# Kernel optimization log

Hardware: AMD Instinct MI355X
Metric: run time of the kernel (lower is better)

## Reference

```python
import jax, jax.numpy as jnp
import numpy as np

B = 524288      # batch
D = 16          # ds_dim
N = 32          # number of dynamical systems
H = 128         # gating hidden width


def setup_inputs() -> dict:
    key = jax.random.key(0)
    ks = jax.random.split(key, 8)
    x_cur = jax.random.normal(ks[0], (B, D), dtype=jnp.float32)
    W1 = jax.random.normal(ks[1], (H, D), dtype=jnp.float32) * 0.1
    b1 = jax.random.normal(ks[2], (H,), dtype=jnp.float32) * 0.1
    W2 = jax.random.normal(ks[3], (N, H), dtype=jnp.float32) * 0.1
    b2 = jax.random.normal(ks[4], (N,), dtype=jnp.float32) * 0.1
    # B matrices are PSD (geotorch.positive_semidefinite), C are skew-symmetric (geotorch.skew)
    Braw = jax.random.normal(ks[5], (N, D, D), dtype=jnp.float32) * 0.3
    B_mats = jnp.einsum('nij,nkj->nik', Braw, Braw)  # PSD: R R^T
    Craw = jax.random.normal(ks[6], (N, D, D), dtype=jnp.float32) * 0.3
    C_mats = 0.5 * (Craw - jnp.swapaxes(Craw, -1, -2))  # skew-symmetric
    x_target = jax.random.normal(ks[7], (1, D), dtype=jnp.float32)
    return {"x_cur": x_cur, "W1": W1, "b1": b1, "W2": W2, "b2": b2,
            "B_mats": B_mats, "C_mats": C_mats, "x_target": x_target}


def reference(x_cur, W1, b1, W2, b2, B_mats, C_mats, x_target):
    # gating weights: softmax(Linear -> ReLU -> Linear)
    h = jax.nn.relu(x_cur @ W1.T + b1)          # [B, H]
    w_all = jax.nn.softmax(h @ W2.T + b2, axis=1)  # [B, N]
    # per-system linear map A_i = B_i + C_i applied to (x* - x)
    A = B_mats + C_mats                          # [N, D, D]
    diff = x_target - x_cur                      # [B, D]
    # torch.mm(A, diff.T).T == diff @ A.T -> proj[b,n,k] = sum_d A[n,k,d] diff[b,d]
    proj = jnp.einsum('nkd,bd->bnk', A, diff)    # [B, N, D]
    out = jnp.einsum('bn,bnk->bk', w_all, proj)  # [B, D]
    return out
```

## Files before the change

kernel.cpp:

```cpp
#include <hip/hip_runtime.h>

#define BATCH 524288

typedef __bf16 bf16x8 __attribute__((ext_vector_type(8)));
typedef __bf16 bf16x2 __attribute__((ext_vector_type(2)));
typedef float f32x4 __attribute__((ext_vector_type(4)));
typedef float f32x8 __attribute__((ext_vector_type(8)));
typedef float f32x2 __attribute__((ext_vector_type(2)));

#define SW1 16384
#define SZC 20480
#define SW2 20512
#define SB2 28704
#define SXT 28832
#define SHC 28896
#define SMEM_BYTES (28896 + 4 * 2560)

__device__ __forceinline__ f32x8 load8(const float* __restrict__ p) {
    float4 a = *(const float4*)p;
    float4 b = *(const float4*)(p + 4);
    f32x8 v = {a.x, a.y, a.z, a.w, b.x, b.y, b.z, b.w};
    return v;
}

__device__ __forceinline__ int pack2bf(float a, float b) {
    f32x2 v = {a, b};
    bf16x2 p = __builtin_convertvector(v, bf16x2);
    return __builtin_bit_cast(int, p);
}

__global__ __launch_bounds__(256, 4) void andp_v10(
    const float* __restrict__ x_cur,
    const float* __restrict__ W1,
    const float* __restrict__ b1,
    const float* __restrict__ W2,
    const float* __restrict__ b2,
    const float* __restrict__ Bm,
    const float* __restrict__ Cm,
    const float* __restrict__ x_t,
    float* __restrict__ out)
{
    extern __shared__ char smem[];
    int* sA2i = (int*)smem;
    int* sW1i = (int*)(smem + SW1);
    int* sW2i = (int*)(smem + SW2);
    const int tid = threadIdx.x;

#pragma unroll
    for (int i = 0; i < 16; ++i) {
        int o2 = tid + i * 256;
        int o  = o2 * 2;
        int kk = o >> 9, qp = (o >> 7) & 3, k = (o >> 3) & 15, j = o & 7;
        int n = 2 * kk + (qp >> 1), d = (qp & 1) * 8 + j;
        int src = n * 256 + k * 16 + d;
        float2 bv = *(const float2*)(Bm + src);
        float2 cv = *(const float2*)(Cm + src);
        sA2i[o2] = pack2bf(bv.x + cv.x, bv.y + cv.y);
    }
#pragma unroll
    for (int i = 0; i < 4; ++i) {
        int o2 = tid + i * 256;
        int o  = o2 * 2;
        int t = o >> 8, qq = (o >> 7) & 1, cc = (o >> 3) & 15, j = o & 7;
        int src = (t * 16 + cc) * 16 + qq * 8 + j;
        float2 v = *(const float2*)(W1 + src);
        sW1i[o2] = pack2bf(v.x, v.y);
    }
    if (tid < 8) ((int*)(smem + SZC))[tid] = 0;
#pragma unroll
    for (int i = 0; i < 8; ++i) {
        int o2 = tid + i * 256;
        int chunk = o2 >> 8, rem = o2 & 255;
        int ln = rem >> 2, j2 = rem & 3;
        int qq = ln >> 4, cc = ln & 15;
        int t2 = chunk >> 2, s = chunk & 3;
        int src = (t2 * 16 + cc) * 128 + s * 32 + 4 * qq + j2;
        sW2i[o2] = pack2bf(W2[src], W2[src + 16]);
    }
    if (tid < 32) ((float*)(smem + SB2))[tid] = b2[tid];
    if (tid < 16) ((float*)(smem + SXT))[tid] = x_t[tid];

    const int wave = tid >> 6, lane = tid & 63;
    const int c = lane & 15, q = lane >> 4;
    const int qh = q >> 1;
    const int hh = (q & 1) * 8;
    const int c4 = c * 4;

    const char* sW1f = smem + SW1;
    const int w1base = (q < 2) ? ((q * 16 + c) * 16) : (SZC - SW1);
    const int w1step = (q < 2) ? 512 : 0;
    const char* sW2f = smem + SW2 + lane * 16;
    __bf16* hcw0 = (__bf16*)(smem + SHC + wave * 2560);
    __bf16* hcw1 = hcw0 + 640;
    const float* sB2f = (const float*)(smem + SB2);
    const float* sXTf = (const float*)(smem + SXT);

    float b1v[8];
#pragma unroll
    for (int t = 0; t < 8; ++t) b1v[t] = b1[t * 16 + c];

    __syncthreads();

    const int blk_row = blockIdx.x * 256 + wave * 64;
    const f32x4 z4 = {0.f, 0.f, 0.f, 0.f};

#pragma unroll 1
    for (int p = 0; p < 2; ++p) {
        const int r0 = blk_row + p * 32;

        bf16x8 af[2];
#pragma unroll
        for (int t01 = 0; t01 < 2; ++t01) {
            f32x8 xv = load8(x_cur + (size_t)(r0 + t01 * 16 + c) * 16 + hh);
            af[t01] = __builtin_convertvector(xv, bf16x8);
        }

        f32x4 acc2[2][2];
        acc2[0][0] = z4; acc2[0][1] = z4; acc2[1][0] = z4; acc2[1][1] = z4;
#pragma unroll
        for (int s = 0; s < 4; ++s) {
#pragma unroll
            for (int t01 = 0; t01 < 2; ++t01) {
                __bf16* hcw = t01 ? hcw1 : hcw0;
                bf16x8 w1a = *(const bf16x8*)(sW1f + w1base + (2 * s) * w1step);
                bf16x8 w1b = *(const bf16x8*)(sW1f + w1base + (2 * s + 1) * w1step);
                f32x4 a1a = __builtin_amdgcn_mfma_f32_16x16x32_bf16(af[t01], w1a, z4, 0, 0, 0);
                f32x4 a1b = __builtin_amdgcn_mfma_f32_16x16x32_bf16(af[t01], w1b, z4, 0, 0, 0);
#pragma unroll
                for (int r = 0; r < 4; ++r) {
                    float va = fmaxf(a1a[r] + b1v[2 * s], 0.f);
                    float vb = fmaxf(a1b[r] + b1v[2 * s + 1], 0.f);
                    *(int*)(hcw + (q * 4 + r) * 40 + 2 * c) = pack2bf(va, vb);
                }
            }
#pragma unroll
            for (int t01 = 0; t01 < 2; ++t01) {
                __bf16* hcw = t01 ? hcw1 : hcw0;
                bf16x8 hb = *(const bf16x8*)(hcw + c * 40 + q * 8);
                bf16x8 w20 = *(const bf16x8*)(sW2f + (0 * 4 + s) * 1024);
                bf16x8 w21 = *(const bf16x8*)(sW2f + (1 * 4 + s) * 1024);
                acc2[t01][0] = __builtin_amdgcn_mfma_f32_16x16x32_bf16(w20, hb, acc2[t01][0], 0, 0, 0);
                acc2[t01][1] = __builtin_amdgcn_mfma_f32_16x16x32_bf16(w21, hb, acc2[t01][1], 0, 0, 0);
            }
        }

        int wq[8];
        {
            f32x4 bq0 = *(const f32x4*)(sB2f + q * 4);
            f32x4 bq1 = *(const f32x4*)(sB2f + 16 + q * 4);
#pragma unroll
            for (int t01 = 0; t01 < 2; ++t01) {
                float e[8], sum = 0.f;
#pragma unroll
                for (int r = 0; r < 4; ++r) {
                    e[r]     = __expf(acc2[t01][0][r] + bq0[r]);
                    e[4 + r] = __expf(acc2[t01][1][r] + bq1[r]);
                    sum += e[r] + e[4 + r];
                }
                sum += __shfl_xor(sum, 16, 64);
                sum += __shfl_xor(sum, 32, 64);
                float inv = 1.0f / sum;
                if (t01 == 0) {
#pragma unroll
                    for (int i = 0; i < 8; ++i) wq[i] = pack2bf(e[i] * inv, 0.f);
                } else {
#pragma unroll
                    for (int i = 0; i < 8; ++i) wq[i] |= pack2bf(0.f, e[i] * inv);
                }
            }
        }

        f32x8 dif[2];
        {
            f32x4 xta = *(const f32x4*)(sXTf + hh);
            f32x4 xtb = *(const f32x4*)(sXTf + hh + 4);
            f32x8 xtv = {xta[0], xta[1], xta[2], xta[3], xtb[0], xtb[1], xtb[2], xtb[3]};
            dif[0] = xtv - __builtin_convertvector(af[0], f32x8);
            dif[1] = xtv - __builtin_convertvector(af[1], f32x8);
        }

        f32x4 acc3[2];
        acc3[0] = z4; acc3[1] = z4;
#pragma unroll
        for (int kk = 0; kk < 16; ++kk) {
            const int lo = (kk >> 3) * 4 + 2 * (kk & 1);
            const int bpi = c4 + ((kk >> 1) & 3) * 64;
            int bpA = __builtin_amdgcn_ds_bpermute(bpi, wq[lo]);
            int bpB = __builtin_amdgcn_ds_bpermute(bpi, wq[lo + 1]);
            int sel = qh ? bpB : bpA;
            float w0 = __builtin_bit_cast(float, (unsigned)sel << 16);
            float w1 = __builtin_bit_cast(float, (unsigned)sel & 0xffff0000u);
            bf16x8 a2f = *(const bf16x8*)(smem + kk * 1024 + lane * 16);
            bf16x8 g0 = __builtin_convertvector(dif[0] * w0, bf16x8);
            bf16x8 g1 = __builtin_convertvector(dif[1] * w1, bf16x8);
            acc3[0] = __builtin_amdgcn_mfma_f32_16x16x32_bf16(a2f, g0, acc3[0], 0, 0, 0);
            acc3[1] = __builtin_amdgcn_mfma_f32_16x16x32_bf16(a2f, g1, acc3[1], 0, 0, 0);
        }

#pragma unroll
        for (int t01 = 0; t01 < 2; ++t01) {
            float4 st = make_float4(acc3[t01][0], acc3[t01][1], acc3[t01][2], acc3[t01][3]);
            *(float4*)(out + (size_t)(r0 + t01 * 16 + c) * 16 + q * 4) = st;
        }
    }
}

extern "C" void kernel_launch(void* const* d_in, const int* in_sizes, int n_in,
                              void* d_out, int out_size, void* d_ws, size_t ws_size,
                              hipStream_t stream) {
    const float* x_cur = (const float*)d_in[0];
    const float* W1    = (const float*)d_in[1];
    const float* b1    = (const float*)d_in[2];
    const float* W2    = (const float*)d_in[3];
    const float* b2    = (const float*)d_in[4];
    const float* Bm    = (const float*)d_in[5];
    const float* Cm    = (const float*)d_in[6];
    const float* x_t   = (const float*)d_in[7];
    float* out = (float*)d_out;

    const int blocks = BATCH / 256;
    andp_v10<<<blocks, 256, SMEM_BYTES, stream>>>(
        x_cur, W1, b1, W2, b2, Bm, Cm, x_t, out);
}
```

Before: 119.5 us.

## Software-pipeline gating MFMAs and prefetch bpermute/LDS loads in mixing loop

Restructures the gating MLP loop so the second-layer MFMAs for step s-1 are issued after the first-layer MFMAs for step s, overlapping LDS hidden round-trips with matrix work. The second-layer bias is folded into the accumulator initialisation. The softmax handles both row tiles together and interleaves their shuffles. The final mixing loop prefetches the next iteration's bpermutes and A-matrix LDS load one step ahead. This raises register pressure under the 4-wave launch bound, and correctness depends on the hidden tile written each step being read before the next step overwrites it.

```diff
diff --git a/kernel.cpp b/kernel.cpp
--- a/kernel.cpp
+++ b/kernel.cpp
@@ -29,7 +29,7 @@
     return __builtin_bit_cast(int, p);
 }
 
-__global__ __launch_bounds__(256, 4) void andp_v10(
+__global__ __launch_bounds__(256, 4) void andp_v11(
     const float* __restrict__ x_cur,
     const float* __restrict__ W1,
     const float* __restrict__ b1,
@@ -115,59 +115,79 @@
             af[t01] = __builtin_convertvector(xv, bf16x8);
         }
 
+        f32x4 bq0 = *(const f32x4*)(sB2f + q * 4);
+        f32x4 bq1 = *(const f32x4*)(sB2f + 16 + q * 4);
         f32x4 acc2[2][2];
-        acc2[0][0] = z4; acc2[0][1] = z4; acc2[1][0] = z4; acc2[1][1] = z4;
+        acc2[0][0] = bq0; acc2[0][1] = bq1;
+        acc2[1][0] = bq0; acc2[1][1] = bq1;
+
+        bf16x8 hbp[2];
 #pragma unroll
         for (int s = 0; s < 4; ++s) {
+            bf16x8 w2a, w2b;
+            if (s > 0) {
+                w2a = *(const bf16x8*)(sW2f + (s - 1) * 1024);
+                w2b = *(const bf16x8*)(sW2f + (4 + s - 1) * 1024);
+            }
+            bf16x8 w1a = *(const bf16x8*)(sW1f + w1base + (2 * s) * w1step);
+            bf16x8 w1b = *(const bf16x8*)(sW1f + w1base + (2 * s + 1) * w1step);
+            f32x4 a1[2][2];
+#pragma unroll
+            for (int t01 = 0; t01 < 2; ++t01) {
+                a1[t01][0] = __builtin_amdgcn_mfma_f32_16x16x32_bf16(af[t01], w1a, z4, 0, 0, 0);
+                a1[t01][1] = __builtin_amdgcn_mfma_f32_16x16x32_bf16(af[t01], w1b, z4, 0, 0, 0);
+            }
+            if (s > 0) {
+#pragma unroll
+                for (int t01 = 0; t01 < 2; ++t01) {
+                    acc2[t01][0] = __builtin_amdgcn_mfma_f32_16x16x32_bf16(w2a, hbp[t01], acc2[t01][0], 0, 0, 0);
+                    acc2[t01][1] = __builtin_amdgcn_mfma_f32_16x16x32_bf16(w2b, hbp[t01], acc2[t01][1], 0, 0, 0);
+                }
+            }
 #pragma unroll
             for (int t01 = 0; t01 < 2; ++t01) {
                 __bf16* hcw = t01 ? hcw1 : hcw0;
-                bf16x8 w1a = *(const bf16x8*)(sW1f + w1base + (2 * s) * w1step);
-                bf16x8 w1b = *(const bf16x8*)(sW1f + w1base + (2 * s + 1) * w1step);
-                f32x4 a1a = __builtin_amdgcn_mfma_f32_16x16x32_bf16(af[t01], w1a, z4, 0, 0, 0);
-                f32x4 a1b = __builtin_amdgcn_mfma_f32_16x16x32_bf16(af[t01], w1b, z4, 0, 0, 0);
 #pragma unroll
                 for (int r = 0; r < 4; ++r) {
-                    float va = fmaxf(a1a[r] + b1v[2 * s], 0.f);
-                    float vb = fmaxf(a1b[r] + b1v[2 * s + 1], 0.f);
+                    float va = fmaxf(a1[t01][0][r] + b1v[2 * s], 0.f);
+                    float vb = fmaxf(a1[t01][1][r] + b1v[2 * s + 1], 0.f);
                     *(int*)(hcw + (q * 4 + r) * 40 + 2 * c) = pack2bf(va, vb);
                 }
             }
+            hbp[0] = *(const bf16x8*)(hcw0 + c * 40 + q * 8);
+            hbp[1] = *(const bf16x8*)(hcw1 + c * 40 + q * 8);
+        }
+        {
+            bf16x8 w2a = *(const bf16x8*)(sW2f + 3 * 1024);
+            bf16x8 w2b = *(const bf16x8*)(sW2f + 7 * 1024);
 #pragma unroll
             for (int t01 = 0; t01 < 2; ++t01) {
-                __bf16* hcw = t01 ? hcw1 : hcw0;
-                bf16x8 hb = *(const bf16x8*)(hcw + c * 40 + q * 8);
-                bf16x8 w20 = *(const bf16x8*)(sW2f + (0 * 4 + s) * 1024);
-                bf16x8 w21 = *(const bf16x8*)(sW2f + (1 * 4 + s) * 1024);
-                acc2[t01][0] = __builtin_amdgcn_mfma_f32_16x16x32_bf16(w20, hb, acc2[t01][0], 0, 0, 0);
-                acc2[t01][1] = __builtin_amdgcn_mfma_f32_16x16x32_bf16(w21, hb, acc2[t01][1], 0, 0, 0);
+                acc2[t01][0] = __builtin_amdgcn_mfma_f32_16x16x32_bf16(w2a, hbp[t01], acc2[t01][0], 0, 0, 0);
+                acc2[t01][1] = __builtin_amdgcn_mfma_f32_16x16x32_bf16(w2b, hbp[t01], acc2[t01][1], 0, 0, 0);
             }
         }
 
         int wq[8];
         {
-            f32x4 bq0 = *(const f32x4*)(sB2f + q * 4);
-            f32x4 bq1 = *(const f32x4*)(sB2f + 16 + q * 4);
-#pragma unroll
-            for (int t01 = 0; t01 < 2; ++t01) {
-                float e[8], sum = 0.f;
+            float e0[8], e1[8];
+            float s0 = 0.f, s1 = 0.f;
+#pragma unroll
+            for (int t2 = 0; t2 < 2; ++t2)
 #pragma unroll
                 for (int r = 0; r < 4; ++r) {
-                    e[r]     = __expf(acc2[t01][0][r] + bq0[r]);
-                    e[4 + r] = __expf(acc2[t01][1][r] + bq1[r]);
-                    sum += e[r] + e[4 + r];
+                    e0[t2 * 4 + r] = __expf(acc2[0][t2][r]);
+                    e1[t2 * 4 + r] = __expf(acc2[1][t2][r]);
+                    s0 += e0[t2 * 4 + r];
+                    s1 += e1[t2 * 4 + r];
                 }
-                sum += __shfl_xor(sum, 16, 64);
-                sum += __shfl_xor(sum, 32, 64);
-                float inv = 1.0f / sum;
-                if (t01 == 0) {
-#pragma unroll
-                    for (int i = 0; i < 8; ++i) wq[i] = pack2bf(e[i] * inv, 0.f);
-                } else {
-#pragma unroll
-                    for (int i = 0; i < 8; ++i) wq[i] |= pack2bf(0.f, e[i] * inv);
-                }
-            }
+            s0 += __shfl_xor(s0, 16, 64);
+            s1 += __shfl_xor(s1, 16, 64);
+            s0 += __shfl_xor(s0, 32, 64);
+            s1 += __shfl_xor(s1, 32, 64);
+            float i0 = 1.0f / s0, i1 = 1.0f / s1;
+#pragma unroll
+            for (int i = 0; i < 8; ++i)
+                wq[i] = pack2bf(e0[i] * i0, e1[i] * i1);
         }
 
         f32x8 dif[2];
@@ -181,20 +201,26 @@
 
         f32x4 acc3[2];
         acc3[0] = z4; acc3[1] = z4;
+        int bpA = __builtin_amdgcn_ds_bpermute(c4 + 0, wq[0]);
+        int bpB = __builtin_amdgcn_ds_bpermute(c4 + 0, wq[1]);
+        bf16x8 a2c = *(const bf16x8*)(smem + 0 * 1024 + lane * 16);
 #pragma unroll
         for (int kk = 0; kk < 16; ++kk) {
-            const int lo = (kk >> 3) * 4 + 2 * (kk & 1);
-            const int bpi = c4 + ((kk >> 1) & 3) * 64;
-            int bpA = __builtin_amdgcn_ds_bpermute(bpi, wq[lo]);
-            int bpB = __builtin_amdgcn_ds_bpermute(bpi, wq[lo + 1]);
-            int sel = qh ? bpB : bpA;
-            float w0 = __builtin_bit_cast(float, (unsigned)sel << 16);
-            float w1 = __builtin_bit_cast(float, (unsigned)sel & 0xffff0000u);
-            bf16x8 a2f = *(const bf16x8*)(smem + kk * 1024 + lane * 16);
+            int selv = qh ? bpB : bpA;
+            bf16x8 a2u = a2c;
+            if (kk < 15) {
+                const int lo = ((kk + 1) >> 3) * 4 + 2 * ((kk + 1) & 1);
+                const int bpi = c4 + (((kk + 1) >> 1) & 3) * 64;
+                bpA = __builtin_amdgcn_ds_bpermute(bpi, wq[lo]);
+                bpB = __builtin_amdgcn_ds_bpermute(bpi, wq[lo + 1]);
+                a2c = *(const bf16x8*)(smem + (kk + 1) * 1024 + lane * 16);
+            }
+            float w0 = __builtin_bit_cast(float, (unsigned)selv << 16);
+            float w1 = __builtin_bit_cast(float, (unsigned)selv & 0xffff0000u);
             bf16x8 g0 = __builtin_convertvector(dif[0] * w0, bf16x8);
             bf16x8 g1 = __builtin_convertvector(dif[1] * w1, bf16x8);
-            acc3[0] = __builtin_amdgcn_mfma_f32_16x16x32_bf16(a2f, g0, acc3[0], 0, 0, 0);
-            acc3[1] = __builtin_amdgcn_mfma_f32_16x16x32_bf16(a2f, g1, acc3[1], 0, 0, 0);
+            acc3[0] = __builtin_amdgcn_mfma_f32_16x16x32_bf16(a2u, g0, acc3[0], 0, 0, 0);
+            acc3[1] = __builtin_amdgcn_mfma_f32_16x16x32_bf16(a2u, g1, acc3[1], 0, 0, 0);
         }
 
 #pragma unroll
@@ -219,6 +245,6 @@
     float* out = (float*)d_out;
 
     const int blocks = BATCH / 256;
-    andp_v10<<<blocks, 256, SMEM_BYTES, stream>>>(
+    andp_v11<<<blocks, 256, SMEM_BYTES, stream>>>(
         x_cur, W1, b1, W2, b2, Bm, Cm, x_t, out);
 }
```

New measurement: 121.5 us. Within noise of the previous version (+1.7%).
